# Performance work log

Hardware: AMD Instinct MI355X
Metric: run time of the kernel (lower is better)

Reference implementation:

```python
import jax, jax.numpy as jnp
import numpy as np

B, H, W = 4, 64, 64
C_IN, C_OUT = 512, 19
INTER = C_IN // 4          # 128
QK = INTER // 8            # 16
BN_EPS = 1e-3              # keras BatchNormalization default epsilon


def setup_inputs() -> dict:
    key = jax.random.key(0)
    ks = jax.random.split(key, 40)
    it = iter(range(40))

    def n(shape, s=0.05):
        return jax.random.normal(ks[next(it)], shape, jnp.float32) * s

    def bnp():
        g = 1.0 + n((INTER,), 0.1)
        b = n((INTER,), 0.1)
        m = n((INTER,), 0.1)
        v = jax.random.uniform(ks[next(it)], (INTER,), jnp.float32, 0.5, 1.5)
        return g, b, m, v

    inp = {"x": jax.random.normal(ks[next(it)], (B, H, W, C_IN), jnp.float32)}
    inp["w5a"] = n((3, 3, C_IN, INTER))
    inp["bn1_g"], inp["bn1_b"], inp["bn1_m"], inp["bn1_v"] = bnp()
    inp["wq"] = n((1, 1, INTER, QK)); inp["bq"] = n((QK,))
    inp["wk"] = n((1, 1, INTER, QK)); inp["bk"] = n((QK,))
    inp["wv"] = n((1, 1, INTER, INTER)); inp["bv"] = n((INTER,))
    inp["gamma_pam"] = jnp.float32(0.7)
    inp["w5c"] = n((3, 3, C_IN, INTER))
    inp["bn2_g"], inp["bn2_b"], inp["bn2_m"], inp["bn2_v"] = bnp()
    inp["gamma_cam"] = jnp.float32(0.6)
    inp["w51"] = n((3, 3, INTER, INTER))
    inp["bn3_g"], inp["bn3_b"], inp["bn3_m"], inp["bn3_v"] = bnp()
    inp["w52"] = n((3, 3, INTER, INTER))
    inp["bn4_g"], inp["bn4_b"], inp["bn4_m"], inp["bn4_v"] = bnp()
    inp["w8"] = n((1, 1, INTER, C_OUT))
    return inp


def _conv(x, w):
    return jax.lax.conv_general_dilated(
        x, w, (1, 1), 'SAME', dimension_numbers=('NHWC', 'HWIO', 'NHWC'))


def _bn(x, g, b, m, v):
    return (x - m) * jax.lax.rsqrt(v + BN_EPS) * g + b


def _danet_fwd(x, w5a, bn1_g, bn1_b, bn1_m, bn1_v, wq, bq, wk, bk, wv, bv,
               gamma_pam, w5c, bn2_g, bn2_b, bn2_m, bn2_v, gamma_cam,
               w51, bn3_g, bn3_b, bn3_m, bn3_v, w52, bn4_g, bn4_b, bn4_m, bn4_v, w8):
    relu = jax.nn.relu
    # --- position-attention branch ---
    feat1 = relu(_bn(_conv(x, w5a), bn1_g, bn1_b, bn1_m, bn1_v))   # [B,H,W,INTER]
    b_, h_, w_, c_ = feat1.shape
    N = h_ * w_
    q = (_conv(feat1, wq) + bq).reshape(b_, N, QK)                 # [B,N,QK]
    kk = (_conv(feat1, wk) + bk).reshape(b_, N, QK)
    vv = (_conv(feat1, wv) + bv).reshape(b_, N, c_)                # [B,N,C]
    att = jax.nn.softmax(jnp.einsum('biq,bjq->bij', q, kk), axis=-1)  # [B,N,N]
    pam = gamma_pam * jnp.einsum('bij,bjc->bic', att, vv).reshape(b_, h_, w_, c_) + feat1
    sa_conv = relu(_bn(_conv(pam, w51), bn3_g, bn3_b, bn3_m, bn3_v))
    # --- channel-attention branch ---
    feat2 = relu(_bn(_conv(x, w5c), bn2_g, bn2_b, bn2_m, bn2_v))
    xc = feat2.reshape(b_, N, c_)                                  # [B,N,C]
    energy = jnp.einsum('bnc,bnd->bcd', xc, xc)                    # [B,C,C]
    energy_new = jnp.max(energy, axis=-1, keepdims=True) - energy
    attc = jax.nn.softmax(energy_new, axis=-1)                     # [B,C,C]
    outc = jnp.einsum('bcd,bnd->bnc', attc, xc)
    cam = gamma_cam * outc.reshape(b_, h_, w_, c_) + feat2
    sc_conv = relu(_bn(_conv(cam, w52), bn4_g, bn4_b, bn4_m, bn4_v))
    # --- fusion (dropout is identity at inference) ---
    return _conv(sa_conv + sc_conv, w8)                            # [B,H,W,C_OUT]


def reference(x, w5a, bn1_g, bn1_b, bn1_m, bn1_v, wq, bq, wk, bk, wv, bv,
              gamma_pam, w5c, bn2_g, bn2_b, bn2_m, bn2_v, gamma_cam,
              w51, bn3_g, bn3_b, bn3_m, bn3_v, w52, bn4_g, bn4_b, bn4_m, bn4_v, w8):
    return _danet_fwd(x, w5a, bn1_g, bn1_b, bn1_m, bn1_v, wq, bq, wk, bk, wv, bv,
                      gamma_pam, w5c, bn2_g, bn2_b, bn2_m, bn2_v, gamma_cam,
                      w51, bn3_g, bn3_b, bn3_m, bn3_v, w52, bn4_g, bn4_b, bn4_m, bn4_v, w8)
```

## Files before the change

kernel.cpp:

```cpp
#include <hip/hip_runtime.h>

typedef unsigned short u16;
typedef unsigned int   u32;
typedef _Float16 f16;
typedef f16   f16x8 __attribute__((ext_vector_type(8)));
typedef float f32x4 __attribute__((ext_vector_type(4)));
typedef u16   u16x8 __attribute__((ext_vector_type(8)));
typedef u16   u16x4 __attribute__((ext_vector_type(4)));
typedef u32   u32x4 __attribute__((ext_vector_type(4)));

#define DI __device__ __forceinline__

DI u16  f2h(float f){ f16 h = (f16)f; return __builtin_bit_cast(u16, h); }
DI float h2f(u16 u){ return (float)__builtin_bit_cast(f16, u); }
DI float hlo(u32 u){ return (float)__builtin_bit_cast(f16, (u16)(u & 0xFFFFu)); }
DI float hhi(u32 u){ return (float)__builtin_bit_cast(f16, (u16)(u >> 16)); }

DI f32x4 MFMA(f16x8 a, f16x8 b, f32x4 c){
  return __builtin_amdgcn_mfma_f32_16x16x32_f16(a, b, c, 0, 0, 0);
}

DI u32 pk2(float lo, float hi){
  typedef __fp16 hf16x2 __attribute__((ext_vector_type(2)));
  hf16x2 r = __builtin_amdgcn_cvt_pkrtz(lo, hi);
  return __builtin_bit_cast(u32, r);
}

DI float dot8h(uint4 a, uint4 b){
  float s;
  s  = hlo(a.x)*hlo(b.x) + hhi(a.x)*hhi(b.x);
  s += hlo(a.y)*hlo(b.y) + hhi(a.y)*hhi(b.y);
  s += hlo(a.z)*hlo(b.z) + hhi(a.z)*hhi(b.z);
  s += hlo(a.w)*hlo(b.w) + hhi(a.w)*hhi(b.w);
  return s;
}

constexpr size_t O_XB    = 0;
constexpr size_t O_F1    = O_XB    + 16777216;
constexpr size_t O_F2H   = O_F1    + 4194304;
constexpr size_t O_F2TH  = O_F2H   + 8388608;
constexpr size_t O_ENP   = O_F2TH  + 4194304;
constexpr size_t O_Q     = O_ENP   + 4194304;
constexpr size_t O_K     = O_Q     + 1048576;
constexpr size_t O_VT    = O_K     + 1048576;
constexpr size_t O_PAM   = O_VT    + 4194304;
constexpr size_t O_CAM   = O_PAM   + 4194304;
constexpr size_t O_EN    = O_CAM   + 4194304;
constexpr size_t O_ATTC  = O_EN    + 262144;
constexpr size_t O_W5AT  = O_ATTC  + 262144;
constexpr size_t O_W5CT  = O_W5AT  + 1179648;
constexpr size_t O_W51T  = O_W5CT  + 1179648;
constexpr size_t O_W52T  = O_W51T  + 294912;
constexpr size_t O_WQT   = O_W52T  + 294912;
constexpr size_t O_WKT   = O_WQT   + 4096;
constexpr size_t O_WVT   = O_WKT   + 4096;
constexpr size_t O_W8T   = O_WVT   + 32768;
constexpr size_t O_B1    = O_W8T   + 8192;
constexpr size_t O_B2    = O_B1    + 512;
constexpr size_t O_B3    = O_B2    + 512;
constexpr size_t O_B4    = O_B3    + 512;
constexpr size_t O_SA    = O_XB;
constexpr size_t O_SC    = O_XB    + 4194304;
constexpr size_t O_OP    = O_XB;
constexpr size_t O_ML    = O_F2TH;
constexpr size_t OP_SPLIT_STRIDE = 2097152;
constexpr size_t ML_SPLIT_STRIDE = 32768;

DI void prep_w3_dev(int idx, const float* __restrict__ w, const float* __restrict__ g,
                    const float* __restrict__ bb, const float* __restrict__ m,
                    const float* __restrict__ v, u16* __restrict__ wT,
                    float* __restrict__ bias, int CIN, int lg2){
  const int n = idx & 127;
  const int rest = idx >> 7;
  const int c = rest & (CIN-1);
  const int t = rest >> lg2;
  const float s = g[n] * rsqrtf(v[n] + 1e-3f);
  wT[((size_t)(t*128 + n))*CIN + c] = f2h(w[idx] * s);
  if(rest == 0) bias[n] = bb[n] - m[n]*s;
}

DI void prep_wt_dev(int idx, const float* __restrict__ w, u16* __restrict__ wt, int K, int N){
  if(idx >= K*N) return;
  const int n = idx % N, k = idx / N;
  wt[n*K + k] = f2h(w[idx]);
}

__global__ void prep_all_k(
    const float* __restrict__ x, u16* __restrict__ xh,
    const float* w5a, const float* g1, const float* b1, const float* m1, const float* v1, u16* W5AT, float* B1,
    const float* w5c, const float* g2, const float* b2, const float* m2, const float* v2, u16* W5CT, float* B2,
    const float* w51, const float* g3, const float* b3, const float* m3, const float* v3, u16* W51T, float* B3,
    const float* w52, const float* g4, const float* b4, const float* m4, const float* v4, u16* W52T, float* B4,
    const float* wq, u16* WQT, const float* wk, u16* WKT,
    const float* wv, u16* WVT, const float* w8, u16* W8T)
{
  int bx = blockIdx.x;
  const int t = threadIdx.x;
  if(bx < 8192){
    const int i = (bx*256 + t)*4;
    const float4 v = *(const float4*)(x + i);
    xh[i] = f2h(v.x); xh[i+1] = f2h(v.y); xh[i+2] = f2h(v.z); xh[i+3] = f2h(v.w);
    return;
  }
  bx -= 8192;
  if(bx < 2304){ prep_w3_dev(bx*256+t, w5a, g1,b1,m1,v1, W5AT, B1, 512, 9); return; }
  bx -= 2304;
  if(bx < 2304){ prep_w3_dev(bx*256+t, w5c, g2,b2,m2,v2, W5CT, B2, 512, 9); return; }
  bx -= 2304;
  if(bx < 576){ prep_w3_dev(bx*256+t, w51, g3,b3,m3,v3, W51T, B3, 128, 7); return; }
  bx -= 576;
  if(bx < 576){ prep_w3_dev(bx*256+t, w52, g4,b4,m4,v4, W52T, B4, 128, 7); return; }
  bx -= 576;
  if(bx < 8){ prep_wt_dev(bx*256+t, wq, WQT, 128, 16); return; }
  bx -= 8;
  if(bx < 8){ prep_wt_dev(bx*256+t, wk, WKT, 128, 16); return; }
  bx -= 8;
  if(bx < 64){ prep_wt_dev(bx*256+t, wv, WVT, 128, 128); return; }
  bx -= 64;
  prep_wt_dev(bx*256+t, w8, W8T, 128, 19);
}

template<int CIN>
__global__ __launch_bounds__(512) void conv3x3_k(
    const u16* __restrict__ ina, const u16* __restrict__ wTa,
    const float* __restrict__ ba, u16* oha, u16* otha,
    const u16* __restrict__ inb, const u16* __restrict__ wTb,
    const float* __restrict__ bb, u16* ohb, u16* othb)
{
  __shared__ __align__(16) char SMEM[73728];

  constexpr int CPS = CIN/64;
  constexpr int S   = 9*CPS;

  const int halfsel = blockIdx.x >> 7;
  const int blk = blockIdx.x & 127;
  const u16* in  = halfsel ? inb : ina;
  const u16* wT  = halfsel ? wTb : wTa;
  const float* bias = halfsel ? bb : ba;
  u16* oh  = halfsel ? ohb : oha;
  u16* oth = halfsel ? othb : otha;

  const int tid = threadIdx.x;
  const int lane = tid & 63;
  const int wid = tid >> 6;
  const int kg = wid >> 2;
  const int wq = wid & 3;
  const int wr = wq >> 1, wc = wq & 1;
  const int l15 = lane & 15;
  const int lg = lane >> 4;
  const int rowS = tid >> 2;
  const int cst  = (tid & 3) * 16;

  const int p = blk*128 + rowS;
  const int b = p >> 12;
  const int rem = p & 4095;
  const int h = rem >> 6, w = rem & 63;

  f32x4 acc[4][4];
  #pragma unroll
  for(int i=0;i<4;++i)
    #pragma unroll
    for(int j=0;j<4;++j){ f32x4 z = {0.f,0.f,0.f,0.f}; acc[i][j] = z; }

  u16x8 ra0, ra1, rb0, rb1;
  auto LOAD = [&](int ts){
    const int tap = ts / CPS;
    const int c0 = (ts - tap*CPS)*64;
    const int dy = tap/3 - 1, dx = tap - (tap/3)*3 - 1;
    const int hh = h + dy, ww = w + dx;
    const bool valid = ((unsigned)hh < 64u) && ((unsigned)ww < 64u);
    u16x8 z = {0,0,0,0,0,0,0,0};
    ra0 = z; ra1 = z;
    if(valid){
      const u16* sp = in + (size_t)((b<<12) + (hh<<6) + ww)*CIN + c0 + cst;
      ra0 = *(const u16x8*)(sp);
      ra1 = *(const u16x8*)(sp + 8);
    }
    const u16* bp = wT + (size_t)(tap*128 + rowS)*CIN + c0 + cst;
    rb0 = *(const u16x8*)(bp);
    rb1 = *(const u16x8*)(bp + 8);
  };
  auto STORE = [&](int buf){
    u16* Ad = (u16*)(SMEM + (buf ? 18432 : 0)) + rowS*72 + cst;
    u16* Bd = (u16*)(SMEM + 36864 + (buf ? 18432 : 0)) + rowS*72 + cst;
    *(u16x8*)(Ad)     = ra0;
    *(u16x8*)(Ad + 8) = ra1;
    *(u16x8*)(Bd)     = rb0;
    *(u16x8*)(Bd + 8) = rb1;
  };

  LOAD(0); STORE(0);
  LOAD(1);
  __syncthreads();

  int cur = 0;
  const int fro = kg*32 + lg*8;
  for(int ts=0; ts<S; ++ts){
    if(ts+1 < S) STORE(cur^1);
    if(ts+2 < S) LOAD(ts+2);
    const u16* Ac = (u16*)(SMEM + (cur ? 18432 : 0));
    const u16* Bc = (u16*)(SMEM + 36864 + (cur ? 18432 : 0));
    f16x8 af[4], bf[4];
    #pragma unroll
    for(int ms=0; ms<4; ++ms)
      af[ms] = *(const f16x8*)(Ac + (wr*64 + ms*16 + l15)*72 + fro);
    #pragma unroll
    for(int ns=0; ns<4; ++ns)
      bf[ns] = *(const f16x8*)(Bc + (wc*64 + ns*16 + l15)*72 + fro);
    #pragma unroll
    for(int ms=0; ms<4; ++ms)
      #pragma unroll
      for(int ns=0; ns<4; ++ns)
        acc[ms][ns] = MFMA(af[ms], bf[ns], acc[ms][ns]);
    __syncthreads();
    cur ^= 1;
  }

  float* Mg = (float*)SMEM + wq*4096;
  if(kg){
    #pragma unroll
    for(int ms=0; ms<4; ++ms)
      #pragma unroll
      for(int ns=0; ns<4; ++ns)
        #pragma unroll
        for(int r=0; r<4; ++r)
          Mg[(ms*16 + lg*4 + r)*64 + ns*16 + l15] = acc[ms][ns][r];
  }
  __syncthreads();
  if(!kg){
    const int orow0 = blk*128 + wr*64;
    #pragma unroll
    for(int ns=0; ns<4; ++ns){
      const int col = wc*64 + ns*16 + l15;
      const float bc = bias[col];
      #pragma unroll
      for(int ms=0; ms<4; ++ms){
        const int pr0 = orow0 + ms*16 + lg*4;
        float4 vv;
        vv.x = acc[ms][ns][0] + Mg[(ms*16+lg*4+0)*64 + ns*16+l15] + bc; vv.x = vv.x > 0.f ? vv.x : 0.f;
        vv.y = acc[ms][ns][1] + Mg[(ms*16+lg*4+1)*64 + ns*16+l15] + bc; vv.y = vv.y > 0.f ? vv.y : 0.f;
        vv.z = acc[ms][ns][2] + Mg[(ms*16+lg*4+2)*64 + ns*16+l15] + bc; vv.z = vv.z > 0.f ? vv.z : 0.f;
        vv.w = acc[ms][ns][3] + Mg[(ms*16+lg*4+3)*64 + ns*16+l15] + bc; vv.w = vv.w > 0.f ? vv.w : 0.f;
        const u16 h0 = f2h(vv.x), h1 = f2h(vv.y), h2 = f2h(vv.z), h3 = f2h(vv.w);
        if(oh){
          oh[(size_t)(pr0+0)*128 + col] = h0;
          oh[(size_t)(pr0+1)*128 + col] = h1;
          oh[(size_t)(pr0+2)*128 + col] = h2;
          oh[(size_t)(pr0+3)*128 + col] = h3;
        }
        if(oth){
          const int bb2 = pr0 >> 12, pp0 = pr0 & 4095;
          u16x4 hv = {h0, h1, h2, h3};
          *(u16x4*)(oth + (size_t)(bb2*128 + col)*4096 + pp0) = hv;
        }
      }
    }
  }
}

__global__ void qk_proj_k(const u16* __restrict__ feat,
                          const u16* __restrict__ wtq, const float* __restrict__ biasq,
                          const u16* __restrict__ wtk, const float* __restrict__ biask,
                          u16* __restrict__ outq, u16* __restrict__ outk){
  const int idx = blockIdx.x*256 + threadIdx.x;
  if(idx >= 16384*16) return;
  const int n = idx & 15, p = idx >> 4;
  const u16* fr = feat + (size_t)p*128;
  const u16* wrq = wtq + n*128;
  const u16* wrk = wtk + n*128;
  float accq = biasq[n], acck = biask[n];
  #pragma unroll
  for(int k=0; k<128; k+=8){
    const uint4 f = *(const uint4*)(fr+k);
    accq += dot8h(f, *(const uint4*)(wrq+k));
    acck += dot8h(f, *(const uint4*)(wrk+k));
  }
  outq[(size_t)p*32 + n] = f2h(accq);
  outq[(size_t)p*32 + 16 + n] = 0;
  outk[(size_t)p*32 + n] = f2h(acck);
  outk[(size_t)p*32 + 16 + n] = 0;
}

__global__ __launch_bounds__(256) void v_proj_mfma_k(
    const u16* __restrict__ feat, const u16* __restrict__ wt,
    const float* __restrict__ bias, u16* __restrict__ vT)
{
  __shared__ u16 Ct[128*136];
  const int b = blockIdx.x >> 5, pb = blockIdx.x & 31;
  const int p0 = pb*128;
  const int tid = threadIdx.x;
  const int lane = tid & 63;
  const int wid = tid >> 6;
  const int wr = wid >> 1, wc = wid & 1;
  const int l15 = lane & 15;
  const int lg = lane >> 4;

  f32x4 acc[4][4];
  #pragma unroll
  for(int i=0;i<4;++i)
    #pragma unroll
    for(int j=0;j<4;++j){ f32x4 z = {0.f,0.f,0.f,0.f}; acc[i][j] = z; }

  #pragma unroll
  for(int k0=0; k0<128; k0+=32){
    f16x8 af[4], bf[4];
    #pragma unroll
    for(int ms=0; ms<4; ++ms)
      af[ms] = *(const f16x8*)(wt + (size_t)(wr*64 + ms*16 + l15)*128 + k0 + lg*8);
    #pragma unroll
    for(int ns=0; ns<4; ++ns)
      bf[ns] = *(const f16x8*)(feat + (size_t)(b*4096 + p0 + wc*64 + ns*16 + l15)*128 + k0 + lg*8);
    #pragma unroll
    for(int ms=0; ms<4; ++ms)
      #pragma unroll
      for(int ns=0; ns<4; ++ns)
        acc[ms][ns] = MFMA(af[ms], bf[ns], acc[ms][ns]);
  }
  #pragma unroll
  for(int ms=0; ms<4; ++ms){
    const int n0 = wr*64 + ms*16 + lg*4;
    #pragma unroll
    for(int r=0; r<4; ++r){
      const float bc = bias[n0 + r];
      #pragma unroll
      for(int ns=0; ns<4; ++ns)
        Ct[(n0+r)*136 + wc*64 + ns*16 + l15] = f2h(acc[ms][ns][r] + bc);
    }
  }
  __syncthreads();
  const int row = tid >> 1, half = tid & 1;
  u16* dst = vT + (size_t)(b*128 + row)*4096 + p0 + half*64;
  const u16* src = Ct + row*136 + half*64;
  #pragma unroll
  for(int j=0; j<8; ++j)
    *(u16x8*)(dst + j*8) = *(const u16x8*)(src + j*8);
}

__global__ __launch_bounds__(512) void pam_part_k(
    const u16* __restrict__ q, const u16* __restrict__ km,
    const u16* __restrict__ vT,
    u16* __restrict__ OP, float* __restrict__ ML)
{
  __shared__ u16 Vl[128*136];
  __shared__ u16 Kl[128*40];
  __shared__ u32 Pp[8*16*66];

  const int tid = threadIdx.x;
  const int lane = tid & 63;
  const int wv = tid >> 6;
  const int l15 = lane & 15;
  const int lg = lane >> 4;
  const int koff = lg*8;
  const int qt = blockIdx.x;
  const int b = blockIdx.y;
  const int ks = blockIdx.z;
  const int q0 = qt*256;

  u32* Pw = Pp + wv*16*66;

  const int row4 = tid >> 2, seg = tid & 3;
  const u16* vsrc = vT + (size_t)(b*128 + row4)*4096 + ks*1024 + seg*32;
  const u16* ksrc = km + (size_t)(b*4096 + ks*1024 + row4)*32 + seg*8;
  u16* vdst = Vl + row4*136 + seg*32;
  u16* kdst = Kl + row4*40 + seg*8;

  f16x8 aQ[2];
  #pragma unroll
  for(int f=0; f<2; ++f)
    aQ[f] = *(const f16x8*)(q + (size_t)(b*4096 + q0 + wv*32 + f*16 + l15)*32 + koff);

  float m_r[2] = {-1e30f, -1e30f};
  float l_r[2] = {0.f, 0.f};

  f32x4 accO[8][2];
  #pragma unroll
  for(int i=0;i<8;++i)
    #pragma unroll
    for(int f=0;f<2;++f){ f32x4 z = {0.f,0.f,0.f,0.f}; accO[i][f] = z; }

  u16x8 rv[4], rk;
  #pragma unroll
  for(int j=0;j<4;++j) rv[j] = *(const u16x8*)(vsrc + j*8);
  rk = *(const u16x8*)(ksrc);
  #pragma unroll
  for(int j=0;j<4;++j) *(u16x8*)(vdst + j*8) = rv[j];
  *(u16x8*)(kdst) = rk;
  __syncthreads();

  const int NT = 8;
  for(int t=0; t<NT; ++t){
    if(t+1 < NT){
      vsrc += 128; ksrc += 128*32;
      #pragma unroll
      for(int j=0;j<4;++j) rv[j] = *(const u16x8*)(vsrc + j*8);
      rk = *(const u16x8*)(ksrc);
    }
    f32x4 accST[8][2];
    #pragma unroll
    for(int ns=0; ns<8; ++ns){
      const f16x8 aK = *(const f16x8*)(Kl + (ns*16 + l15)*40 + koff);
      f32x4 z = {0.f,0.f,0.f,0.f};
      accST[ns][0] = MFMA(aK, aQ[0], z);
      accST[ns][1] = MFMA(aK, aQ[1], z);
    }
    float al_[2];
    #pragma unroll
    for(int f=0; f<2; ++f){
      float tmax = accST[0][f][0];
      #pragma unroll
      for(int ns=0; ns<8; ++ns)
        #pragma unroll
        for(int ri=0; ri<4; ++ri) tmax = fmaxf(tmax, accST[ns][f][ri]);
      tmax = fmaxf(tmax, __shfl_xor(tmax, 16));
      tmax = fmaxf(tmax, __shfl_xor(tmax, 32));
      const float mn = fmaxf(m_r[f], tmax);
      const float al = __expf(m_r[f] - mn);
      float ps = 0.f;
      #pragma unroll
      for(int ns=0; ns<8; ++ns)
        #pragma unroll
        for(int ri=0; ri<4; ++ri){
          const float pv = __expf(accST[ns][f][ri] - mn);
          accST[ns][f][ri] = pv;
          ps += pv;
        }
      ps += __shfl_xor(ps, 16);
      ps += __shfl_xor(ps, 32);
      l_r[f] = l_r[f]*al + ps;
      m_r[f] = mn;
      al_[f] = al;
    }
    #pragma unroll
    for(int ns2=0; ns2<8; ++ns2)
      #pragma unroll
      for(int f=0; f<2; ++f)
        #pragma unroll
        for(int ri=0; ri<4; ++ri)
          accO[ns2][f][ri] *= al_[f];
    #pragma unroll
    for(int f=0; f<2; ++f){
      #pragma unroll
      for(int ns=0; ns<8; ++ns){
        uint2 pr;
        pr.x = pk2(accST[ns][f][0], accST[ns][f][1]);
        pr.y = pk2(accST[ns][f][2], accST[ns][f][3]);
        *(uint2*)(Pw + l15*66 + ns*8 + lg*2) = pr;
      }
      #pragma unroll
      for(int kk=0; kk<4; ++kk){
        const uint2 ra = *(const uint2*)(Pw + l15*66 + kk*16 + lg*4);
        const uint2 rb = *(const uint2*)(Pw + l15*66 + kk*16 + lg*4 + 2);
        u32x4 rr; rr.x = ra.x; rr.y = ra.y; rr.z = rb.x; rr.w = rb.y;
        const f16x8 bP = __builtin_bit_cast(f16x8, rr);
        #pragma unroll
        for(int ns2=0; ns2<8; ++ns2){
          const f16x8 av = *(const f16x8*)(Vl + (ns2*16 + l15)*136 + kk*32 + koff);
          accO[ns2][f] = MFMA(av, bP, accO[ns2][f]);
        }
      }
    }
    __syncthreads();
    if(t+1 < NT){
      #pragma unroll
      for(int j=0;j<4;++j) *(u16x8*)(vdst + j*8) = rv[j];
      *(u16x8*)(kdst) = rk;
      __syncthreads();
    }
  }

  u32* op32 = (u32*)(OP + (size_t)ks*OP_SPLIT_STRIDE + (size_t)(b*16 + qt)*32768);
  #pragma unroll
  for(int f=0; f<2; ++f){
    const int ql = wv*32 + f*16 + l15;
    #pragma unroll
    for(int ns2=0; ns2<8; ++ns2)
      #pragma unroll
      for(int h=0; h<2; ++h)
        op32[ql*64 + ns2*8 + lg*2 + h] = pk2(accO[ns2][f][2*h], accO[ns2][f][2*h+1]);
  }
  float* ml = ML + (size_t)ks*ML_SPLIT_STRIDE + (size_t)(b*16 + qt)*512;
  if(lg == 0){
    #pragma unroll
    for(int f=0; f<2; ++f){
      const int ql = wv*32 + f*16 + l15;
      ml[ql*2]     = m_r[f];
      ml[ql*2 + 1] = l_r[f];
    }
  }
}

__global__ void pam_merge_k(const u16* __restrict__ OP, const float* __restrict__ ML,
                            const u16* __restrict__ feat1, const float* __restrict__ gpam,
                            u16* __restrict__ pam)
{
  const int idx = blockIdx.x*256 + threadIdx.x;
  const int ch = idx & 127, qg = idx >> 7;
  const int b = qg >> 12, qq = qg & 4095;
  const int qt = qq >> 8, ql = qq & 255;
  const size_t off = ((size_t)(b*16 + qt)*256 + ql)*128 + ch;
  const size_t mloff = (size_t)(b*16 + qt)*512 + ql*2;
  float m[4], l[4];
  #pragma unroll
  for(int s=0; s<4; ++s){
    m[s] = ML[s*ML_SPLIT_STRIDE + mloff];
    l[s] = ML[s*ML_SPLIT_STRIDE + mloff + 1];
  }
  const float M = fmaxf(fmaxf(m[0],m[1]), fmaxf(m[2],m[3]));
  float num = 0.f, den = 0.f;
  #pragma unroll
  for(int s=0; s<4; ++s){
    const float wgt = __expf(m[s] - M);
    num += wgt * h2f(OP[s*OP_SPLIT_STRIDE + off]);
    den += wgt * l[s];
  }
  pam[idx] = f2h(gpam[0]*num/den + h2f(feat1[idx]));
}

__global__ __launch_bounds__(256) void energy_mfma_k(const u16* __restrict__ f2T,
                                                     float* __restrict__ enp){
  __shared__ u16 Xl[128*72];
  const int b = blockIdx.x >> 4, s = blockIdx.x & 15;
  const int tid = threadIdx.x;
  const int lane = tid & 63;
  const int wid = tid >> 6;
  const int wr = wid >> 1, wc = wid & 1;
  const int l15 = lane & 15;
  const int lg = lane >> 4;
  const int rowS = tid >> 1, half = tid & 1;
  const u16* src = f2T + (size_t)(b*128 + rowS)*4096 + s*256;

  f32x4 acc[4][4];
  #pragma unroll
  for(int i=0;i<4;++i)
    #pragma unroll
    for(int j=0;j<4;++j){ f32x4 z = {0.f,0.f,0.f,0.f}; acc[i][j] = z; }

  for(int it=0; it<4; ++it){
    __syncthreads();
    const u16* sp = src + it*64 + half*32;
    const u16x8 v0 = *(const u16x8*)(sp);
    const u16x8 v1 = *(const u16x8*)(sp + 8);
    const u16x8 v2 = *(const u16x8*)(sp + 16);
    const u16x8 v3 = *(const u16x8*)(sp + 24);
    u16* dl = Xl + rowS*72 + half*32;
    *(u16x8*)(dl)      = v0;
    *(u16x8*)(dl + 8)  = v1;
    *(u16x8*)(dl + 16) = v2;
    *(u16x8*)(dl + 24) = v3;
    __syncthreads();
    #pragma unroll
    for(int kk=0; kk<2; ++kk){
      f16x8 af[4], bf[4];
      #pragma unroll
      for(int ms=0; ms<4; ++ms)
        af[ms] = *(const f16x8*)(Xl + (wr*64 + ms*16 + l15)*72 + kk*32 + lg*8);
      #pragma unroll
      for(int ns=0; ns<4; ++ns)
        bf[ns] = *(const f16x8*)(Xl + (wc*64 + ns*16 + l15)*72 + kk*32 + lg*8);
      #pragma unroll
      for(int ms=0; ms<4; ++ms)
        #pragma unroll
        for(int ns=0; ns<4; ++ns)
          acc[ms][ns] = MFMA(af[ms], bf[ns], acc[ms][ns]);
    }
  }
  float* dst = enp + (size_t)(s*4 + b)*128*128;
  #pragma unroll
  for(int ms=0; ms<4; ++ms){
    const int r0 = wr*64 + ms*16 + lg*4;
    #pragma unroll
    for(int ns=0; ns<4; ++ns){
      const int col = wc*64 + ns*16 + l15;
      #pragma unroll
      for(int r=0; r<4; ++r)
        dst[(size_t)(r0 + r)*128 + col] = acc[ms][ns][r];
    }
  }
}

__global__ __launch_bounds__(256) void attc_k(const float* __restrict__ enp, u16* __restrict__ attch){
  const int row = blockIdx.x*4 + (threadIdx.x >> 6);
  const int lane = threadIdx.x & 63;
  float e0 = 0.f, e1 = 0.f;
  const int b = row >> 7, c = row & 127;
  #pragma unroll
  for(int s=0; s<16; ++s){
    const float* base = enp + (size_t)(s*4 + b)*128*128 + (size_t)c*128;
    e0 += base[lane];
    e1 += base[64 + lane];
  }
  float mn = fminf(e0, e1);
  #pragma unroll
  for(int d2=1; d2<64; d2<<=1) mn = fminf(mn, __shfl_xor(mn, d2));
  const float p0 = __expf(mn - e0), p1 = __expf(mn - e1);
  float s = p0 + p1;
  #pragma unroll
  for(int d2=1; d2<64; d2<<=1) s += __shfl_xor(s, d2);
  const float rs = 1.f / s;
  attch[(size_t)row*128 + lane]      = f2h(p0*rs);
  attch[(size_t)row*128 + 64 + lane] = f2h(p1*rs);
}

__global__ __launch_bounds__(256) void cam_mfma_k(
    const u16* __restrict__ f2, const u16* __restrict__ attch,
    const float* __restrict__ gcam, u16* __restrict__ cam)
{
  const int b = blockIdx.x >> 5, pt = blockIdx.x & 31;
  const int tid = threadIdx.x;
  const int lane = tid & 63;
  const int wid = tid >> 6;
  const int wr = wid >> 1, wc = wid & 1;
  const int l15 = lane & 15;
  const int lg = lane >> 4;

  f32x4 acc[4][4];
  #pragma unroll
  for(int i=0;i<4;++i)
    #pragma unroll
    for(int j=0;j<4;++j){ f32x4 z = {0.f,0.f,0.f,0.f}; acc[i][j] = z; }

  #pragma unroll
  for(int k0=0; k0<128; k0+=32){
    f16x8 af[4], bf[4];
    #pragma unroll
    for(int ms=0; ms<4; ++ms)
      af[ms] = *(const f16x8*)(f2 + (size_t)(b*4096 + pt*128 + wr*64 + ms*16 + l15)*128 + k0 + lg*8);
    #pragma unroll
    for(int ns=0; ns<4; ++ns)
      bf[ns] = *(const f16x8*)(attch + (size_t)(b*128 + wc*64 + ns*16 + l15)*128 + k0 + lg*8);
    #pragma unroll
    for(int ms=0; ms<4; ++ms)
      #pragma unroll
      for(int ns=0; ns<4; ++ns)
        acc[ms][ns] = MFMA(af[ms], bf[ns], acc[ms][ns]);
  }
  const float g = gcam[0];
  #pragma unroll
  for(int ms=0; ms<4; ++ms)
    #pragma unroll
    for(int ns=0; ns<4; ++ns){
      const int col = wc*64 + ns*16 + l15;
      #pragma unroll
      for(int r=0; r<4; ++r){
        const int p = pt*128 + wr*64 + ms*16 + lg*4 + r;
        const size_t off = (size_t)(b*4096 + p)*128 + col;
        cam[off] = f2h(g*acc[ms][ns][r] + h2f(f2[off]));
      }
    }
}

__global__ void final_k(const u16* __restrict__ sa, const u16* __restrict__ sc,
                        const u16* __restrict__ w8t, float* __restrict__ out){
  const int idx = blockIdx.x*256 + threadIdx.x;
  if(idx >= 16384*19) return;
  const int p = idx / 19, n = idx - p*19;
  const u16* ra = sa + (size_t)p*128;
  const u16* rb = sc + (size_t)p*128;
  const u16* wr = w8t + (size_t)n*128;
  float acc = 0.f;
  #pragma unroll
  for(int k=0; k<128; k+=8){
    const uint4 a = *(const uint4*)(ra+k);
    const uint4 b = *(const uint4*)(rb+k);
    const uint4 w = *(const uint4*)(wr+k);
    acc += (hlo(a.x)+hlo(b.x))*hlo(w.x) + (hhi(a.x)+hhi(b.x))*hhi(w.x);
    acc += (hlo(a.y)+hlo(b.y))*hlo(w.y) + (hhi(a.y)+hhi(b.y))*hhi(w.y);
    acc += (hlo(a.z)+hlo(b.z))*hlo(w.z) + (hhi(a.z)+hhi(b.z))*hhi(w.z);
    acc += (hlo(a.w)+hlo(b.w))*hlo(w.w) + (hhi(a.w)+hhi(b.w))*hhi(w.w);
  }
  out[idx] = acc;
}

extern "C" void kernel_launch(void* const* d_in, const int* in_sizes, int n_in,
                              void* d_out, int out_size, void* d_ws, size_t ws_size,
                              hipStream_t stream)
{
  const float* x    = (const float*)d_in[0];
  const float* w5a  = (const float*)d_in[1];
  const float* bn1g = (const float*)d_in[2];
  const float* bn1b = (const float*)d_in[3];
  const float* bn1m = (const float*)d_in[4];
  const float* bn1v = (const float*)d_in[5];
  const float* wq   = (const float*)d_in[6];
  const float* bq   = (const float*)d_in[7];
  const float* wk   = (const float*)d_in[8];
  const float* bk   = (const float*)d_in[9];
  const float* wv   = (const float*)d_in[10];
  const float* bv   = (const float*)d_in[11];
  const float* gpam = (const float*)d_in[12];
  const float* w5c  = (const float*)d_in[13];
  const float* bn2g = (const float*)d_in[14];
  const float* bn2b = (const float*)d_in[15];
  const float* bn2m = (const float*)d_in[16];
  const float* bn2v = (const float*)d_in[17];
  const float* gcam = (const float*)d_in[18];
  const float* w51  = (const float*)d_in[19];
  const float* bn3g = (const float*)d_in[20];
  const float* bn3b = (const float*)d_in[21];
  const float* bn3m = (const float*)d_in[22];
  const float* bn3v = (const float*)d_in[23];
  const float* w52  = (const float*)d_in[24];
  const float* bn4g = (const float*)d_in[25];
  const float* bn4b = (const float*)d_in[26];
  const float* bn4m = (const float*)d_in[27];
  const float* bn4v = (const float*)d_in[28];
  const float* w8   = (const float*)d_in[29];

  char* ws = (char*)d_ws;
  u16*   XB    = (u16*)(ws + O_XB);
  u16*   FEAT1 = (u16*)(ws + O_F1);
  u16*   F2H   = (u16*)(ws + O_F2H);
  u16*   F2TH  = (u16*)(ws + O_F2TH);
  float* ENP   = (float*)(ws + O_ENP);
  u16*   Q     = (u16*)(ws + O_Q);
  u16*   KM    = (u16*)(ws + O_K);
  u16*   VT    = (u16*)(ws + O_VT);
  u16*   PAM   = (u16*)(ws + O_PAM);
  u16*   CAM   = (u16*)(ws + O_CAM);
  u16*   ATTCH = (u16*)(ws + O_ATTC);
  u16*   OP    = (u16*)(ws + O_OP);
  float* ML    = (float*)(ws + O_ML);
  u16*   W5AT  = (u16*)(ws + O_W5AT);
  u16*   W5CT  = (u16*)(ws + O_W5CT);
  u16*   W51T  = (u16*)(ws + O_W51T);
  u16*   W52T  = (u16*)(ws + O_W52T);
  u16*   WQT   = (u16*)(ws + O_WQT);
  u16*   WKT   = (u16*)(ws + O_WKT);
  u16*   WVT   = (u16*)(ws + O_WVT);
  u16*   W8T   = (u16*)(ws + O_W8T);
  float* B1    = (float*)(ws + O_B1);
  float* B2    = (float*)(ws + O_B2);
  float* B3    = (float*)(ws + O_B3);
  float* B4    = (float*)(ws + O_B4);
  u16*   SA    = (u16*)(ws + O_SA);
  u16*   SC    = (u16*)(ws + O_SC);
  float* OUT   = (float*)d_out;

  prep_all_k<<<14042,256,0,stream>>>(x, XB,
      w5a, bn1g,bn1b,bn1m,bn1v, W5AT, B1,
      w5c, bn2g,bn2b,bn2m,bn2v, W5CT, B2,
      w51, bn3g,bn3b,bn3m,bn3v, W51T, B3,
      w52, bn4g,bn4b,bn4m,bn4v, W52T, B4,
      wq, WQT, wk, WKT, wv, WVT, w8, W8T);

  conv3x3_k<512><<<256,512,0,stream>>>(XB, W5AT, B1, FEAT1, nullptr,
                                       XB, W5CT, B2, F2H, F2TH);

  qk_proj_k<<<1024,256,0,stream>>>(FEAT1, WQT, bq, WKT, bk, Q, KM);
  v_proj_mfma_k<<<128,256,0,stream>>>(FEAT1, WVT, bv, VT);

  energy_mfma_k<<<64,256,0,stream>>>(F2TH, ENP);
  attc_k<<<128,256,0,stream>>>(ENP, ATTCH);
  cam_mfma_k<<<128,256,0,stream>>>(F2H, ATTCH, gcam, CAM);

  pam_part_k<<<dim3(16,4,4),512,0,stream>>>(Q, KM, VT, OP, ML);
  pam_merge_k<<<8192,256,0,stream>>>(OP, ML, FEAT1, gpam, PAM);

  conv3x3_k<128><<<256,512,0,stream>>>(PAM, W51T, B3, SA, nullptr,
                                       CAM, W52T, B4, SC, nullptr);

  final_k<<<1216,256,0,stream>>>(SA, SC, W8T, OUT);
}
```

Baseline: 207.7 us.

## Split-K the 3x3 convolutions across two blocks and merge partials in separate kernels

Each conv3x3 launch now uses a second grid dimension that splits the K loop (taps times channel chunks) into even and odd steps. The two halves write fp16 partial sums to scratch buffers. New merge kernels add the partials, apply bias and ReLU, and write the fp16 and transposed outputs. This doubles the block count from 256 to 512 so more CUs are busy, at the cost of extra global traffic, two extra launches, and the precision loss of rounding partials to fp16.

```diff
diff --git a/kernel.cpp b/kernel.cpp
--- a/kernel.cpp
+++ b/kernel.cpp
@@ -59,8 +59,11 @@
 constexpr size_t O_B2    = O_B1    + 512;
 constexpr size_t O_B3    = O_B2    + 512;
 constexpr size_t O_B4    = O_B3    + 512;
-constexpr size_t O_SA    = O_XB;
-constexpr size_t O_SC    = O_XB    + 4194304;
+constexpr size_t O_CP1   = O_ENP;
+constexpr size_t O_CP2   = O_XB;
+constexpr size_t CP_HALF = 2097152;
+constexpr size_t O_SA    = O_F2TH;
+constexpr size_t O_SC    = O_F2TH + 4194304;
 constexpr size_t O_OP    = O_XB;
 constexpr size_t O_ML    = O_F2TH;
 constexpr size_t OP_SPLIT_STRIDE = 2097152;
@@ -123,9 +126,8 @@
 template<int CIN>
 __global__ __launch_bounds__(512) void conv3x3_k(
     const u16* __restrict__ ina, const u16* __restrict__ wTa,
-    const float* __restrict__ ba, u16* oha, u16* otha,
     const u16* __restrict__ inb, const u16* __restrict__ wTb,
-    const float* __restrict__ bb, u16* ohb, u16* othb)
+    u16* __restrict__ CP)
 {
   __shared__ __align__(16) char SMEM[73728];
 
@@ -134,11 +136,11 @@
 
   const int halfsel = blockIdx.x >> 7;
   const int blk = blockIdx.x & 127;
+  const int ks = blockIdx.y;
+  const int Sk = (S - ks + 1) >> 1;
   const u16* in  = halfsel ? inb : ina;
   const u16* wT  = halfsel ? wTb : wTa;
-  const float* bias = halfsel ? bb : ba;
-  u16* oh  = halfsel ? ohb : oha;
-  u16* oth = halfsel ? othb : otha;
+  u16* op = CP + (size_t)(halfsel*2 + ks)*CP_HALF;
 
   const int tid = threadIdx.x;
   const int lane = tid & 63;
@@ -163,9 +165,9 @@
     for(int j=0;j<4;++j){ f32x4 z = {0.f,0.f,0.f,0.f}; acc[i][j] = z; }
 
   u16x8 ra0, ra1, rb0, rb1;
-  auto LOAD = [&](int ts){
-    const int tap = ts / CPS;
-    const int c0 = (ts - tap*CPS)*64;
+  auto LOAD = [&](int g){
+    const int tap = g / CPS;
+    const int c0 = (g - tap*CPS)*64;
     const int dy = tap/3 - 1, dx = tap - (tap/3)*3 - 1;
     const int hh = h + dy, ww = w + dx;
     const bool valid = ((unsigned)hh < 64u) && ((unsigned)ww < 64u);
@@ -189,15 +191,15 @@
     *(u16x8*)(Bd + 8) = rb1;
   };
 
-  LOAD(0); STORE(0);
-  LOAD(1);
+  LOAD(ks); STORE(0);
+  if(Sk > 1) LOAD(2 + ks);
   __syncthreads();
 
   int cur = 0;
   const int fro = kg*32 + lg*8;
-  for(int ts=0; ts<S; ++ts){
-    if(ts+1 < S) STORE(cur^1);
-    if(ts+2 < S) LOAD(ts+2);
+  for(int ts=0; ts<Sk; ++ts){
+    if(ts+1 < Sk) STORE(cur^1);
+    if(ts+2 < Sk) LOAD(2*(ts+2) + ks);
     const u16* Ac = (u16*)(SMEM + (cur ? 18432 : 0));
     const u16* Bc = (u16*)(SMEM + 36864 + (cur ? 18432 : 0));
     f16x8 af[4], bf[4];
@@ -232,30 +234,91 @@
     #pragma unroll
     for(int ns=0; ns<4; ++ns){
       const int col = wc*64 + ns*16 + l15;
-      const float bc = bias[col];
       #pragma unroll
       for(int ms=0; ms<4; ++ms){
         const int pr0 = orow0 + ms*16 + lg*4;
-        float4 vv;
-        vv.x = acc[ms][ns][0] + Mg[(ms*16+lg*4+0)*64 + ns*16+l15] + bc; vv.x = vv.x > 0.f ? vv.x : 0.f;
-        vv.y = acc[ms][ns][1] + Mg[(ms*16+lg*4+1)*64 + ns*16+l15] + bc; vv.y = vv.y > 0.f ? vv.y : 0.f;
-        vv.z = acc[ms][ns][2] + Mg[(ms*16+lg*4+2)*64 + ns*16+l15] + bc; vv.z = vv.z > 0.f ? vv.z : 0.f;
-        vv.w = acc[ms][ns][3] + Mg[(ms*16+lg*4+3)*64 + ns*16+l15] + bc; vv.w = vv.w > 0.f ? vv.w : 0.f;
-        const u16 h0 = f2h(vv.x), h1 = f2h(vv.y), h2 = f2h(vv.z), h3 = f2h(vv.w);
-        if(oh){
-          oh[(size_t)(pr0+0)*128 + col] = h0;
-          oh[(size_t)(pr0+1)*128 + col] = h1;
-          oh[(size_t)(pr0+2)*128 + col] = h2;
-          oh[(size_t)(pr0+3)*128 + col] = h3;
-        }
-        if(oth){
-          const int bb2 = pr0 >> 12, pp0 = pr0 & 4095;
-          u16x4 hv = {h0, h1, h2, h3};
-          *(u16x4*)(oth + (size_t)(bb2*128 + col)*4096 + pp0) = hv;
+        #pragma unroll
+        for(int r=0; r<4; ++r){
+          const float v = acc[ms][ns][r] + Mg[(ms*16+lg*4+r)*64 + ns*16+l15];
+          op[(size_t)(pr0+r)*128 + col] = f2h(v);
         }
       }
     }
   }
+}
+
+__global__ __launch_bounds__(256) void merge1_k(
+    const u16* __restrict__ CP, const float* __restrict__ B1f, const float* __restrict__ B2f,
+    u16* __restrict__ F1, u16* __restrict__ F2H, u16* __restrict__ F2TH)
+{
+  __shared__ u16 Ct[128*136];
+  const int branchB = blockIdx.x >> 7;
+  const int blk = blockIdx.x & 127;
+  const int tid = threadIdx.x;
+  const u16* P0 = CP + (size_t)(branchB*2 + 0)*CP_HALF + (size_t)blk*16384;
+  const u16* P1 = CP + (size_t)(branchB*2 + 1)*CP_HALF + (size_t)blk*16384;
+  const float* bias = branchB ? B2f : B1f;
+  u16* dsth = (branchB ? F2H : F1) + (size_t)blk*16384;
+
+  #pragma unroll
+  for(int j=0; j<8; ++j){
+    const int e = j*256 + tid;
+    const int off = e*8;
+    const int pl = off >> 7, c0 = off & 127;
+    const u16x8 a = *(const u16x8*)(P0 + off);
+    const u16x8 bb = *(const u16x8*)(P1 + off);
+    const float4 w0 = *(const float4*)(bias + c0);
+    const float4 w1 = *(const float4*)(bias + c0 + 4);
+    float v[8];
+    v[0]=h2f(a[0])+h2f(bb[0])+w0.x; v[1]=h2f(a[1])+h2f(bb[1])+w0.y;
+    v[2]=h2f(a[2])+h2f(bb[2])+w0.z; v[3]=h2f(a[3])+h2f(bb[3])+w0.w;
+    v[4]=h2f(a[4])+h2f(bb[4])+w1.x; v[5]=h2f(a[5])+h2f(bb[5])+w1.y;
+    v[6]=h2f(a[6])+h2f(bb[6])+w1.z; v[7]=h2f(a[7])+h2f(bb[7])+w1.w;
+    u16x8 o;
+    #pragma unroll
+    for(int i=0;i<8;++i){ const float r = v[i] > 0.f ? v[i] : 0.f; o[i] = f2h(r); }
+    *(u16x8*)(dsth + off) = o;
+    if(branchB){
+      #pragma unroll
+      for(int i=0;i<8;++i) Ct[(c0+i)*136 + pl] = o[i];
+    }
+  }
+  if(branchB){
+    __syncthreads();
+    const int row = tid >> 1, half = tid & 1;
+    const int b = blk >> 5, pp0 = (blk & 31)*128;
+    u16* dst = F2TH + (size_t)(b*128 + row)*4096 + pp0 + half*64;
+    const u16* src = Ct + row*136 + half*64;
+    #pragma unroll
+    for(int j=0; j<8; ++j)
+      *(u16x8*)(dst + j*8) = *(const u16x8*)(src + j*8);
+  }
+}
+
+__global__ __launch_bounds__(256) void merge2_k(
+    const u16* __restrict__ CP, const float* __restrict__ B3f, const float* __restrict__ B4f,
+    u16* __restrict__ SA, u16* __restrict__ SC)
+{
+  const int bx = blockIdx.x;
+  const int branch = bx >> 10;
+  const size_t off = ((size_t)(bx & 1023)*256 + threadIdx.x)*8;
+  const u16* P0 = CP + (size_t)(branch*2 + 0)*CP_HALF + off;
+  const u16* P1 = CP + (size_t)(branch*2 + 1)*CP_HALF + off;
+  const float* bias = branch ? B4f : B3f;
+  const int c0 = (int)(off & 127);
+  const u16x8 a = *(const u16x8*)(P0);
+  const u16x8 bb = *(const u16x8*)(P1);
+  const float4 w0 = *(const float4*)(bias + c0);
+  const float4 w1 = *(const float4*)(bias + c0 + 4);
+  float v[8];
+  v[0]=h2f(a[0])+h2f(bb[0])+w0.x; v[1]=h2f(a[1])+h2f(bb[1])+w0.y;
+  v[2]=h2f(a[2])+h2f(bb[2])+w0.z; v[3]=h2f(a[3])+h2f(bb[3])+w0.w;
+  v[4]=h2f(a[4])+h2f(bb[4])+w1.x; v[5]=h2f(a[5])+h2f(bb[5])+w1.y;
+  v[6]=h2f(a[6])+h2f(bb[6])+w1.z; v[7]=h2f(a[7])+h2f(bb[7])+w1.w;
+  u16x8 o;
+  #pragma unroll
+  for(int i=0;i<8;++i){ const float r = v[i] > 0.f ? v[i] : 0.f; o[i] = f2h(r); }
+  *(u16x8*)((branch ? SC : SA) + off) = o;
 }
 
 __global__ void qk_proj_k(const u16* __restrict__ feat,
@@ -720,6 +783,8 @@
   u16*   ATTCH = (u16*)(ws + O_ATTC);
   u16*   OP    = (u16*)(ws + O_OP);
   float* ML    = (float*)(ws + O_ML);
+  u16*   CP1   = (u16*)(ws + O_CP1);
+  u16*   CP2   = (u16*)(ws + O_CP2);
   u16*   W5AT  = (u16*)(ws + O_W5AT);
   u16*   W5CT  = (u16*)(ws + O_W5CT);
   u16*   W51T  = (u16*)(ws + O_W51T);
@@ -743,8 +808,8 @@
       w52, bn4g,bn4b,bn4m,bn4v, W52T, B4,
       wq, WQT, wk, WKT, wv, WVT, w8, W8T);
 
-  conv3x3_k<512><<<256,512,0,stream>>>(XB, W5AT, B1, FEAT1, nullptr,
-                                       XB, W5CT, B2, F2H, F2TH);
+  conv3x3_k<512><<<dim3(256,2),512,0,stream>>>(XB, W5AT, XB, W5CT, CP1);
+  merge1_k<<<256,256,0,stream>>>(CP1, B1, B2, FEAT1, F2H, F2TH);
 
   qk_proj_k<<<1024,256,0,stream>>>(FEAT1, WQT, bq, WKT, bk, Q, KM);
   v_proj_mfma_k<<<128,256,0,stream>>>(FEAT1, WVT, bv, VT);
@@ -756,8 +821,8 @@
   pam_part_k<<<dim3(16,4,4),512,0,stream>>>(Q, KM, VT, OP, ML);
   pam_merge_k<<<8192,256,0,stream>>>(OP, ML, FEAT1, gpam, PAM);
 
-  conv3x3_k<128><<<256,512,0,stream>>>(PAM, W51T, B3, SA, nullptr,
-                                       CAM, W52T, B4, SC, nullptr);
+  conv3x3_k<128><<<dim3(256,2),512,0,stream>>>(PAM, W51T, CAM, W52T, CP2);
+  merge2_k<<<2048,256,0,stream>>>(CP2, B3, B4, SA, SC);
 
   final_k<<<1216,256,0,stream>>>(SA, SC, W8T, OUT);
 }
```

Measured after the change: 218.3 us. +5.1%, slower.
